# Performance work log

Hardware: AMD Instinct MI355X
Metric: run time of the kernel (lower is better)

## Reference

```python
import jax, jax.numpy as jnp
import numpy as np

N, E, M, B = 1024, 8192, 8192, 64
IN_CH, H_CH, H = 512, 1024, 8
D = H_CH // H  # 128


def setup_inputs() -> dict:
    key = jax.random.key(0)
    ks = jax.random.split(key, 16)
    inp = {
        "q": jax.random.normal(ks[0], (N, IN_CH), jnp.float32),
        "k": jax.random.normal(ks[1], (N, IN_CH), jnp.float32),
        "v": jax.random.normal(ks[2], (N, IN_CH), jnp.float32),
        "envelope": jax.random.uniform(ks[3], (M,), jnp.float32),
        "attn_bias": jax.random.normal(ks[4], (N, M), jnp.float32),
        "Wq": jax.random.normal(ks[5], (H_CH, IN_CH), jnp.float32) / np.sqrt(IN_CH),
        "bq": jnp.zeros((H_CH,), jnp.float32),
        "Wk": jax.random.normal(ks[6], (H_CH, IN_CH), jnp.float32) / np.sqrt(IN_CH),
        "bk": jnp.zeros((H_CH,), jnp.float32),
        "Wv": jax.random.normal(ks[7], (H_CH, IN_CH), jnp.float32) / np.sqrt(IN_CH),
        "bv": jnp.zeros((H_CH,), jnp.float32),
        "ln_g": jnp.ones((H_CH,), jnp.float32),
        "ln_b": jnp.zeros((H_CH,), jnp.float32),
        "Wo": jax.random.normal(ks[8], (IN_CH, H_CH), jnp.float32) / np.sqrt(H_CH),
        "bo": jnp.zeros((IN_CH,), jnp.float32),
        "atom_index": jax.random.randint(ks[9], (E,), 0, N),
        "batch_index": jnp.sort(jax.random.randint(ks[10], (E,), 0, B)),
        "edge_map_tab": jax.random.randint(ks[11], (E,), 0, M),
    }
    return inp


def reference(q, k, v, envelope, attn_bias, Wq, bq, Wk, bk, Wv, bv, ln_g, ln_b, Wo, bo,
              atom_index, batch_index, edge_map_tab):
    # projections
    qp = q @ Wq.T + bq                       # [N, H_CH]
    kp = k @ Wk.T + bk
    vp = v @ Wv.T + bv
    # edge gather of k/v
    ke = kp[atom_index].reshape(E, H, D)     # [E, H, D]
    ve = vp[atom_index].reshape(E, H, D)
    qh = qp.reshape(N, H, D)
    # scores: torch computes q*sqrt(d)/d == q/sqrt(d)
    scores = jnp.einsum('nhd,ehd->ehn', qh, ke) / jnp.sqrt(jnp.float32(D))  # [E, H, N]
    scores = scores + attn_bias[:, edge_map_tab].T[:, None, :]             # [E, 1, N]
    env_e = envelope[edge_map_tab]                                          # [E]
    # smooth scatter softmax over edges grouped by batch_index
    seg_max = jax.ops.segment_max(scores, batch_index, num_segments=B)      # [B, H, N]
    ex = jnp.exp(scores - seg_max[batch_index]) * env_e[:, None, None]
    seg_sum = jax.ops.segment_sum(ex, batch_index, num_segments=B)
    w = ex / (seg_sum[batch_index] + 1e-16)
    # second envelope weighting
    w = w * env_e[:, None, None]
    out = jnp.einsum('ehn,ehd->nhd', w, ve).reshape(N, H_CH)
    # layer norm (eps=1e-7)
    mu = out.mean(-1, keepdims=True)
    var = out.var(-1, keepdims=True)
    out = (out - mu) / jnp.sqrt(var + 1e-7) * ln_g + ln_b
    return out @ Wo.T + bo                    # [N, IN_CH]
```

## Files before the change

### kernel.cpp

```cpp
#include <hip/hip_runtime.h>
#include <hip/hip_bf16.h>
#include <math.h>

#define N_ATOMS 1024
#define E_EDGES 8192
#define M_ENV   8192
#define B_SEG   64
#define IN_CH   512
#define H_CH    1024
#define H_HEADS 8
#define D_HEAD  128

typedef __attribute__((ext_vector_type(8))) short short8_t;
typedef __attribute__((ext_vector_type(4))) float f32x4;
typedef __attribute__((ext_vector_type(4))) unsigned short ushort4_t;

__device__ __forceinline__ unsigned short f2bf(float x) {
    union { float f; unsigned u; } c; c.f = x;
    unsigned r = c.u + 0x7FFF + ((c.u >> 16) & 1);
    return (unsigned short)(r >> 16);
}
__device__ __forceinline__ float bf2f(unsigned short b) {
    union { unsigned u; float f; } c; c.u = ((unsigned)b) << 16;
    return c.f;
}

__global__ __launch_bounds__(256) void seg_offsets_k(const int* __restrict__ batch_index,
                                                     int* __restrict__ seg_off) {
    __shared__ int cnt[B_SEG];
    int t = threadIdx.x;
    if (t < B_SEG) cnt[t] = 0;
    __syncthreads();
    for (int e = t; e < E_EDGES; e += 256) {
        atomicAdd(&cnt[batch_index[e]], 1);
    }
    __syncthreads();
    if (t == 0) {
        int acc = 0;
        for (int b = 0; b < B_SEG; ++b) { seg_off[b] = acc; acc += cnt[b]; }
        seg_off[B_SEG] = acc;
    }
}

__global__ __launch_bounds__(256) void pack_k(const int* __restrict__ atom_index,
                                              const int* __restrict__ edge_map,
                                              const int* __restrict__ batch_index,
                                              const float* __restrict__ envelope,
                                              int2* __restrict__ pkenv) {
    const int e = blockIdx.x * 256 + threadIdx.x;
    const int a = atom_index[e];
    const int em = edge_map[e];
    const int bg = batch_index[e];
    int2 o;
    o.x = a | (em << 10) | (bg << 23);
    o.y = __float_as_int(envelope[em]);
    pkenv[e] = o;
}

__global__ __launch_bounds__(256) void transpose_bias_k(const float* __restrict__ ab,
                                                        unsigned short* __restrict__ abT) {
    __shared__ float tile[64][65];
    const int m0 = blockIdx.x * 64;
    const int n0 = blockIdx.y * 64;
    const int t = threadIdx.x;
    const int c4 = (t & 15) * 4;
    const int r  = t >> 4;
#pragma unroll
    for (int it = 0; it < 4; ++it) {
        const int row = r + it * 16;
        const float4 v = *(const float4*)(ab + (size_t)(n0 + row) * M_ENV + m0 + c4);
        tile[row][c4 + 0] = v.x;
        tile[row][c4 + 1] = v.y;
        tile[row][c4 + 2] = v.z;
        tile[row][c4 + 3] = v.w;
    }
    __syncthreads();
    const int mr = t >> 2;
    const int nq = t & 3;
#pragma unroll
    for (int i = 0; i < 4; ++i) {
        const int nl = nq * 4 + i * 16;
        ushort4_t o;
        o[0] = f2bf(tile[nl + 0][mr]);
        o[1] = f2bf(tile[nl + 1][mr]);
        o[2] = f2bf(tile[nl + 2][mr]);
        o[3] = f2bf(tile[nl + 3][mr]);
        *(ushort4_t*)(abT + (size_t)(m0 + mr) * N_ATOMS + n0 + nl) = o;
    }
}

struct Proj3 {
    const float* A[3];
    const float* B[3];
    const float* bia[3];
    unsigned short* C[3];
};

__global__ __launch_bounds__(256) void proj3_k(Proj3 P) {
    __shared__ unsigned short As[64 * 40];
    __shared__ unsigned short Bs[64 * 40];
    const int t = threadIdx.x;
    const int w = t >> 6, lane = t & 63, g = lane >> 4, lo = lane & 15;
    const int m0 = blockIdx.x * 64, n0 = blockIdx.y * 64;
    const int z = blockIdx.z;
    const int srow = t >> 2, sc8 = (t & 3) * 8;
    const float scale = (z == 0) ? 0.08838834764831845f : 1.0f;

    f32x4 acc[4];
#pragma unroll
    for (int nf = 0; nf < 4; ++nf) acc[nf] = (f32x4){0.f, 0.f, 0.f, 0.f};

    const float* gA = P.A[z] + (size_t)(m0 + srow) * IN_CH + sc8;
    const float* gB = P.B[z] + (size_t)(n0 + srow) * IN_CH + sc8;
    const int swr = srow * 40 + sc8;

    for (int k0 = 0; k0 < IN_CH; k0 += 32) {
        const float4 a0 = *(const float4*)(gA + k0);
        const float4 a1 = *(const float4*)(gA + k0 + 4);
        const float4 b0 = *(const float4*)(gB + k0);
        const float4 b1 = *(const float4*)(gB + k0 + 4);
        short8_t av, bvv;
        av[0]=f2bf(a0.x); av[1]=f2bf(a0.y); av[2]=f2bf(a0.z); av[3]=f2bf(a0.w);
        av[4]=f2bf(a1.x); av[5]=f2bf(a1.y); av[6]=f2bf(a1.z); av[7]=f2bf(a1.w);
        bvv[0]=f2bf(b0.x); bvv[1]=f2bf(b0.y); bvv[2]=f2bf(b0.z); bvv[3]=f2bf(b0.w);
        bvv[4]=f2bf(b1.x); bvv[5]=f2bf(b1.y); bvv[6]=f2bf(b1.z); bvv[7]=f2bf(b1.w);
        __syncthreads();
        *(short8_t*)&As[swr] = av;
        *(short8_t*)&Bs[swr] = bvv;
        __syncthreads();
        const short8_t af = *(const short8_t*)&As[(w * 16 + lo) * 40 + g * 8];
#pragma unroll
        for (int nf = 0; nf < 4; ++nf) {
            const short8_t bf = *(const short8_t*)&Bs[(nf * 16 + lo) * 40 + g * 8];
            acc[nf] = __builtin_amdgcn_mfma_f32_16x16x32_bf16(af, bf, acc[nf], 0, 0, 0);
        }
    }

#pragma unroll
    for (int nf = 0; nf < 4; ++nf) {
        const int col = n0 + nf * 16 + lo;
        const float bvv = P.bia[z][col];
#pragma unroll
        for (int r = 0; r < 4; ++r) {
            const int row = m0 + w * 16 + 4 * g + r;
            P.C[z][(size_t)row * H_CH + col] = f2bf((acc[nf][r] + bvv) * scale);
        }
    }
}

__global__ __launch_bounds__(256) void spre_k(const unsigned short* __restrict__ kb,
                                              const unsigned short* __restrict__ qb,
                                              unsigned short* __restrict__ SpT) {
    __shared__ unsigned short As[64 * 40];
    __shared__ unsigned short Bs[64 * 40];
    const int t = threadIdx.x;
    const int w = t >> 6, lane = t & 63, g = lane >> 4, lo = lane & 15;
    const int a0 = blockIdx.x * 64, n0 = blockIdx.y * 64;
    const int h = blockIdx.z;
    const int srow = t >> 2, sc8 = (t & 3) * 8;

    f32x4 acc[4];
#pragma unroll
    for (int nf = 0; nf < 4; ++nf) acc[nf] = (f32x4){0.f, 0.f, 0.f, 0.f};

    const unsigned short* gA = kb + (size_t)(a0 + srow) * H_CH + h * D_HEAD + sc8;
    const unsigned short* gB = qb + (size_t)(n0 + srow) * H_CH + h * D_HEAD + sc8;
    const int swr = srow * 40 + sc8;

#pragma unroll
    for (int k0 = 0; k0 < D_HEAD; k0 += 32) {
        const short8_t av = *(const short8_t*)(gA + k0);
        const short8_t bv = *(const short8_t*)(gB + k0);
        __syncthreads();
        *(short8_t*)&As[swr] = av;
        *(short8_t*)&Bs[swr] = bv;
        __syncthreads();
        const short8_t af = *(const short8_t*)&As[(w * 16 + lo) * 40 + g * 8];
#pragma unroll
        for (int nf = 0; nf < 4; ++nf) {
            const short8_t bf = *(const short8_t*)&Bs[(nf * 16 + lo) * 40 + g * 8];
            acc[nf] = __builtin_amdgcn_mfma_f32_16x16x32_bf16(af, bf, acc[nf], 0, 0, 0);
        }
    }

    unsigned short* dst = SpT + ((size_t)h << 20);
#pragma unroll
    for (int nf = 0; nf < 4; ++nf) {
        const int col = n0 + nf * 16 + lo;
#pragma unroll
        for (int r = 0; r < 4; ++r) {
            const int row = a0 + w * 16 + 4 * g + r;
            dst[(size_t)row * N_ATOMS + col] = f2bf(acc[nf][r]);
        }
    }
}

__global__ __launch_bounds__(256) void lsum3_k(const unsigned short* __restrict__ SpT,
                                               const unsigned short* __restrict__ abT,
                                               const int2* __restrict__ pkenv,
                                               const int* __restrict__ seg_off,
                                               unsigned short* __restrict__ rrbf) {
    __shared__ float lred[16][128];
    const int t = threadIdx.x;
    const int cslot = (t & 15) * 8;
    const int eway = t >> 4;
    const int n0 = blockIdx.x * 128;
    const int h = blockIdx.y, s = blockIdx.z;
    const unsigned short* Sh = SpT + ((size_t)h << 20);

    const int e0 = seg_off[s], e1 = seg_off[s + 1];
    float l[8] = {};

#pragma unroll 2
    for (int e = e0 + eway; e < e1; e += 16) {
        const int2 pk = pkenv[e];
        const float env = __int_as_float(pk.y);
        const int a_  = pk.x & 1023;
        const int em_ = (pk.x >> 10) & 8191;
        const short8_t su = *(const short8_t*)(Sh  + (size_t)a_  * N_ATOMS + n0 + cslot);
        const short8_t bu = *(const short8_t*)(abT + (size_t)em_ * N_ATOMS + n0 + cslot);
#pragma unroll
        for (int j = 0; j < 8; ++j)
            l[j] += __expf(bf2f((unsigned short)su[j]) + bf2f((unsigned short)bu[j])) * env;
    }
#pragma unroll
    for (int j = 0; j < 8; ++j) lred[eway][cslot + j] = l[j];
    __syncthreads();
    if (t < 128) {
        float sum = 0.f;
#pragma unroll
        for (int wv = 0; wv < 16; ++wv) sum += lred[wv][t];
        rrbf[(((size_t)h * B_SEG + s) << 10) + n0 + t] = f2bf(1.0f / (sum + 1e-16f));
    }
}

#define LGKM_BARRIER()                                          \
    do {                                                        \
        asm volatile("s_waitcnt lgkmcnt(0)" ::: "memory");      \
        __builtin_amdgcn_sched_barrier(0);                      \
        __builtin_amdgcn_s_barrier();                           \
    } while (0)

#define PV_GATHER(cc)                                                            \
    do {                                                                         \
        const int eb = ebase + (cc) * 64;                                        \
        _Pragma("unroll")                                                        \
        for (int ei = 0; ei < 2; ++ei) {                                         \
            const int e = eb + ei * 32 + (lane >> 1);                            \
            const int2 pk = pkenv[e];                                            \
            pkP[ei] = pk.x;                                                      \
            enP[ei] = __int_as_float(pk.y);                                      \
            const int a_  = pk.x & 1023;                                         \
            const int em_ = (pk.x >> 10) & 8191;                                 \
            sP[ei] = *(const short8_t*)(Sh  + (size_t)a_  * N_ATOMS + ncol8);    \
            bP[ei] = *(const short8_t*)(abT + (size_t)em_ * N_ATOMS + ncol8);    \
        }                                                                        \
        {                                                                        \
            const int eA = eb + el;                                              \
            const int aA = pkenv[eA].x & 1023;                                   \
            const int aB = pkenv[eA + 1].x & 1023;                               \
            const unsigned short* pA = vh + (size_t)aA * H_CH;                   \
            const unsigned short* pB = vh + (size_t)aB * H_CH;                   \
            vP[0] = *(const short8_t*)(pA);                                      \
            vP[1] = *(const short8_t*)(pA + 8);                                  \
            vP[2] = *(const short8_t*)(pB);                                      \
            vP[3] = *(const short8_t*)(pB + 8);                                  \
        }                                                                        \
    } while (0)

__global__ __launch_bounds__(256, 4) void pv4_k(
    const unsigned short* __restrict__ SpT,
    const unsigned short* __restrict__ vb,
    const unsigned short* __restrict__ abT,
    const int2* __restrict__ pkenv,
    const unsigned short* __restrict__ rrbf,
    unsigned short* __restrict__ part)
{
    __shared__ unsigned short plds[64][72];
    __shared__ unsigned short vst[128][72];
    __shared__ unsigned short rrlds[64 * 64];

    const int t = threadIdx.x;
    const int wid = t >> 6, lane = t & 63;
    const int g = lane >> 4, lo = lane & 15;
    const int half = lane & 1;
    const int n0 = blockIdx.x * 64;
    const int h = blockIdx.y, kc = blockIdx.z;
    const int ebase = kc * 1024;
    const int c8l = wid * 16 + half * 8;
    const int ncol8 = n0 + c8l;
    const unsigned short* Sh = SpT + ((size_t)h << 20);
    const int el = (t & 31) * 2;
    const int dh = (t >> 5) * 16;
    const unsigned short* vh = vb + h * D_HEAD + dh;

    {
        const int s_ = t >> 2;
        const int c16 = (t & 3) * 16;
        const unsigned short* src = rrbf + (((size_t)h * B_SEG + s_) << 10) + n0 + c16;
#pragma unroll
        for (int b2 = 0; b2 < 2; ++b2) {
            const int cb = (t & 3) * 2 + b2;
            const int pos = cb ^ (s_ & 7);
            *(short8_t*)&rrlds[s_ * 64 + pos * 8] = *(const short8_t*)(src + b2 * 8);
        }
    }
    __syncthreads();

    f32x4 osg[8];
#pragma unroll
    for (int di = 0; di < 8; ++di) osg[di] = (f32x4){0.f, 0.f, 0.f, 0.f};

    int pkP[2];
    short8_t sP[2], bP[2];
    float enP[2];
    short8_t vP[4];

    PV_GATHER(0);

    for (int sc = 0; sc < 16; ++sc) {
        LGKM_BARRIER();

#pragma unroll
        for (int j = 0; j < 8; ++j) {
            const int d0 = dh + j;
            const int c0 = ((((el >> 3) ^ (d0 >> 4)) & 7) << 3) + (el & 7);
            *(unsigned*)&vst[d0][c0] =
                (unsigned)(unsigned short)vP[0][j] |
                ((unsigned)(unsigned short)vP[2][j] << 16);
            const int d1 = dh + 8 + j;
            const int c1 = ((((el >> 3) ^ (d1 >> 4)) & 7) << 3) + (el & 7);
            *(unsigned*)&vst[d1][c1] =
                (unsigned)(unsigned short)vP[1][j] |
                ((unsigned)(unsigned short)vP[3][j] << 16);
        }
#pragma unroll
        for (int ei = 0; ei < 2; ++ei) {
            const int bseg = (pkP[ei] >> 23) & 63;
            const int cbr = (wid * 2 + half) ^ (bseg & 7);
            const short8_t rr8 = *(const short8_t*)&rrlds[bseg * 64 + cbr * 8];
            const float ee2 = enP[ei] * enP[ei];
            const int e_loc = ei * 32 + (lane >> 1);
#pragma unroll
            for (int j = 0; j < 8; ++j) {
                const float sv = bf2f((unsigned short)sP[ei][j]) + bf2f((unsigned short)bP[ei][j]);
                const float w_ = __expf(sv) * ee2 * bf2f((unsigned short)rr8[j]);
                plds[c8l + j][e_loc] = f2bf(w_);
            }
        }
        LGKM_BARRIER();

        if (sc + 1 < 16) PV_GATHER(sc + 1);

        const short8_t af0 = *(const short8_t*)&plds[wid * 16 + lo][g * 8];
        const short8_t af1 = *(const short8_t*)&plds[wid * 16 + lo][32 + g * 8];
        __builtin_amdgcn_s_setprio(1);
#pragma unroll
        for (int di = 0; di < 8; ++di) {
            const short8_t b0 = *(const short8_t*)&vst[di * 16 + lo][((g ^ di) & 7) << 3];
            osg[di] = __builtin_amdgcn_mfma_f32_16x16x32_bf16(af0, b0, osg[di], 0, 0, 0);
            const short8_t b1 = *(const short8_t*)&vst[di * 16 + lo][(((4 + g) ^ di) & 7) << 3];
            osg[di] = __builtin_amdgcn_mfma_f32_16x16x32_bf16(af1, b1, osg[di], 0, 0, 0);
        }
        __builtin_amdgcn_s_setprio(0);
    }

#pragma unroll
    for (int di = 0; di < 8; ++di)
#pragma unroll
        for (int r = 0; r < 4; ++r)
            part[((size_t)kc * N_ATOMS + n0 + wid * 16 + 4 * g + r) * H_CH
                 + h * D_HEAD + di * 16 + lo] = f2bf(osg[di][r]);
}

__global__ __launch_bounds__(256) void layernorm8_k(const unsigned short* __restrict__ part,
                                                    const float* __restrict__ gm,
                                                    const float* __restrict__ bt,
                                                    unsigned short* __restrict__ y) {
    const int row = blockIdx.x;
    const int t = threadIdx.x;
    const size_t base = (size_t)row * H_CH;
    float4 v = make_float4(0.f, 0.f, 0.f, 0.f);
#pragma unroll
    for (int p = 0; p < 8; ++p) {
        const ushort4_t a = ((const ushort4_t*)(part + (size_t)p * N_ATOMS * H_CH + base))[t];
        v.x += bf2f(a[0]); v.y += bf2f(a[1]); v.z += bf2f(a[2]); v.w += bf2f(a[3]);
    }

    float s  = v.x + v.y + v.z + v.w;
    float s2 = v.x * v.x + v.y * v.y + v.z * v.z + v.w * v.w;
#pragma unroll
    for (int o = 1; o < 64; o <<= 1) {
        s  += __shfl_xor(s, o);
        s2 += __shfl_xor(s2, o);
    }
    __shared__ float red[8];
    const int wid = t >> 6;
    if ((t & 63) == 0) { red[wid] = s; red[wid + 4] = s2; }
    __syncthreads();
    const float ts  = red[0] + red[1] + red[2] + red[3];
    const float ts2 = red[4] + red[5] + red[6] + red[7];

    const float mean = ts * (1.0f / (float)H_CH);
    const float var  = ts2 * (1.0f / (float)H_CH) - mean * mean;
    const float rstd = rsqrtf(var + 1e-7f);

    const float4 gv = ((const float4*)gm)[t];
    const float4 bv = ((const float4*)bt)[t];
    ushort4_t o;
    o[0] = f2bf((v.x - mean) * rstd * gv.x + bv.x);
    o[1] = f2bf((v.y - mean) * rstd * gv.y + bv.y);
    o[2] = f2bf((v.z - mean) * rstd * gv.z + bv.z);
    o[3] = f2bf((v.w - mean) * rstd * gv.w + bv.w);
    ((ushort4_t*)(y + base))[t] = o;
}

__global__ __launch_bounds__(256) void gemm_out_k(const unsigned short* __restrict__ A,
                                                  const float* __restrict__ B,
                                                  const float* __restrict__ bias,
                                                  float* __restrict__ C) {
    __shared__ unsigned short As[64 * 40];
    __shared__ unsigned short Bs[64 * 40];
    const int t = threadIdx.x;
    const int w = t >> 6, lane = t & 63, g = lane >> 4, lo = lane & 15;
    const int m0 = blockIdx.x * 64, n0 = blockIdx.y * 64;
    const int srow = t >> 2, sc8 = (t & 3) * 8;

    f32x4 acc[4];
#pragma unroll
    for (int nf = 0; nf < 4; ++nf) acc[nf] = (f32x4){0.f, 0.f, 0.f, 0.f};

    const unsigned short* gA = A + (size_t)(m0 + srow) * H_CH + sc8;
    const float* gB = B + (size_t)(n0 + srow) * H_CH + sc8;
    const int swr = srow * 40 + sc8;

    for (int k0 = 0; k0 < H_CH; k0 += 32) {
        const short8_t av = *(const short8_t*)(gA + k0);
        const float4 b0 = *(const float4*)(gB + k0);
        const float4 b1 = *(const float4*)(gB + k0 + 4);
        short8_t bvv;
        bvv[0]=f2bf(b0.x); bvv[1]=f2bf(b0.y); bvv[2]=f2bf(b0.z); bvv[3]=f2bf(b0.w);
        bvv[4]=f2bf(b1.x); bvv[5]=f2bf(b1.y); bvv[6]=f2bf(b1.z); bvv[7]=f2bf(b1.w);
        __syncthreads();
        *(short8_t*)&As[swr] = av;
        *(short8_t*)&Bs[swr] = bvv;
        __syncthreads();
        const short8_t af = *(const short8_t*)&As[(w * 16 + lo) * 40 + g * 8];
#pragma unroll
        for (int nf = 0; nf < 4; ++nf) {
            const short8_t bf = *(const short8_t*)&Bs[(nf * 16 + lo) * 40 + g * 8];
            acc[nf] = __builtin_amdgcn_mfma_f32_16x16x32_bf16(af, bf, acc[nf], 0, 0, 0);
        }
    }

#pragma unroll
    for (int nf = 0; nf < 4; ++nf) {
        const int col = n0 + nf * 16 + lo;
        const float bvv = bias[col];
#pragma unroll
        for (int r = 0; r < 4; ++r) {
            const int row = m0 + w * 16 + 4 * g + r;
            C[(size_t)row * IN_CH + col] = acc[nf][r] + bvv;
        }
    }
}

extern "C" void kernel_launch(void* const* d_in, const int* in_sizes, int n_in,
                              void* d_out, int out_size, void* d_ws, size_t ws_size,
                              hipStream_t stream) {
    (void)in_sizes; (void)n_in; (void)out_size; (void)ws_size;
    const float* q         = (const float*)d_in[0];
    const float* k         = (const float*)d_in[1];
    const float* v         = (const float*)d_in[2];
    const float* envelope  = (const float*)d_in[3];
    const float* attn_bias = (const float*)d_in[4];
    const float* Wq        = (const float*)d_in[5];
    const float* bq        = (const float*)d_in[6];
    const float* Wk        = (const float*)d_in[7];
    const float* bk        = (const float*)d_in[8];
    const float* Wv        = (const float*)d_in[9];
    const float* bv        = (const float*)d_in[10];
    const float* ln_g      = (const float*)d_in[11];
    const float* ln_b      = (const float*)d_in[12];
    const float* Wo        = (const float*)d_in[13];
    const float* bo        = (const float*)d_in[14];
    const int* atom_index  = (const int*)d_in[15];
    const int* batch_index = (const int*)d_in[16];
    const int* edge_map    = (const int*)d_in[17];
    float* out = (float*)d_out;

    char* w8 = (char*)d_ws;
    unsigned short* SpT   = (unsigned short*)(w8);
    unsigned short* abT   = (unsigned short*)(w8 + (16u << 20));
    unsigned short* partb = (unsigned short*)(w8 + (32u << 20));
    unsigned short* vbuf  = (unsigned short*)(w8 + (48u << 20));
    unsigned short* qb    = (unsigned short*)(w8 + (50u << 20));
    unsigned short* kb    = (unsigned short*)(w8 + (52u << 20));
    unsigned short* ln_o  = (unsigned short*)(w8 + (54u << 20));
    unsigned short* rrbf  = (unsigned short*)(w8 + (56u << 20));
    int2*           pkenv = (int2*)          (w8 + (58u << 20));
    int*            seg   = (int*)           (w8 + (59u << 20));

    seg_offsets_k<<<1, 256, 0, stream>>>(batch_index, seg);
    pack_k<<<E_EDGES / 256, 256, 0, stream>>>(atom_index, edge_map, batch_index,
                                              envelope, pkenv);
    transpose_bias_k<<<dim3(M_ENV / 64, N_ATOMS / 64), 256, 0, stream>>>(attn_bias, abT);

    Proj3 pj;
    pj.A[0] = q;   pj.A[1] = k;   pj.A[2] = v;
    pj.B[0] = Wq;  pj.B[1] = Wk;  pj.B[2] = Wv;
    pj.bia[0] = bq; pj.bia[1] = bk; pj.bia[2] = bv;
    pj.C[0] = qb;  pj.C[1] = kb;  pj.C[2] = vbuf;
    proj3_k<<<dim3(16, 16, 3), 256, 0, stream>>>(pj);

    spre_k<<<dim3(16, 16, H_HEADS), 256, 0, stream>>>(kb, qb, SpT);

    lsum3_k<<<dim3(8, H_HEADS, B_SEG), 256, 0, stream>>>(SpT, abT, pkenv, seg, rrbf);

    pv4_k<<<dim3(N_ATOMS / 64, H_HEADS, 8), 256, 0, stream>>>(
        SpT, vbuf, abT, pkenv, rrbf, partb);

    layernorm8_k<<<N_ATOMS, 256, 0, stream>>>(partb, ln_g, ln_b, ln_o);

    gemm_out_k<<<dim3(16, 8), 256, 0, stream>>>(ln_o, Wo, bo, out);
}
```

Before: 170.1 us.

## Double-buffer PV gathers two chunks ahead, swizzle P tile, shuffle V indices

The PV kernel now keeps two register sets of gathered edge data, so each chunk's global loads are issued two chunks before they are consumed rather than one. The P tile in LDS gets an XOR column swizzle to cut bank conflicts on the scattered writes and fragment reads. The atom indices for the V gather are taken by wave shuffles from already loaded pack data instead of reloading pkenv from global memory. The extra register set raises VGPR pressure, which could hurt occupancy under the 4-blocks launch bound.

```diff
diff --git a/kernel.cpp b/kernel.cpp
--- a/kernel.cpp
+++ b/kernel.cpp
@@ -241,34 +241,88 @@
         __builtin_amdgcn_s_barrier();                           \
     } while (0)
 
-#define PV_GATHER(cc)                                                            \
+#define PV_GATHER(pkX, sX, bX, enX, vX, cc)                                      \
     do {                                                                         \
-        const int eb = ebase + (cc) * 64;                                        \
+        const int eb_ = ebase + (cc) * 64;                                       \
         _Pragma("unroll")                                                        \
         for (int ei = 0; ei < 2; ++ei) {                                         \
-            const int e = eb + ei * 32 + (lane >> 1);                            \
+            const int e = eb_ + ei * 32 + (lane >> 1);                           \
             const int2 pk = pkenv[e];                                            \
-            pkP[ei] = pk.x;                                                      \
-            enP[ei] = __int_as_float(pk.y);                                      \
+            pkX[ei] = pk.x;                                                      \
+            enX[ei] = __int_as_float(pk.y);                                      \
             const int a_  = pk.x & 1023;                                         \
             const int em_ = (pk.x >> 10) & 8191;                                 \
-            sP[ei] = *(const short8_t*)(Sh  + (size_t)a_  * N_ATOMS + ncol8);    \
-            bP[ei] = *(const short8_t*)(abT + (size_t)em_ * N_ATOMS + ncol8);    \
+            sX[ei] = *(const short8_t*)(Sh  + (size_t)a_  * N_ATOMS + ncol8);    \
+            bX[ei] = *(const short8_t*)(abT + (size_t)em_ * N_ATOMS + ncol8);    \
         }                                                                        \
         {                                                                        \
-            const int eA = eb + el;                                              \
-            const int aA = pkenv[eA].x & 1023;                                   \
-            const int aB = pkenv[eA + 1].x & 1023;                               \
+              \
+            const int sl0 = (el & 31) * 2;                                       \
+            const int va00 = __shfl(pkX[0], sl0);                                \
+            const int va01 = __shfl(pkX[1], sl0);                                \
+            const int va10 = __shfl(pkX[0], sl0 + 2);                            \
+            const int va11 = __shfl(pkX[1], sl0 + 2);                            \
+            const int aA = ((el < 32) ? va00 : va01) & 1023;                     \
+            const int aB = ((el < 32) ? va10 : va11) & 1023;                     \
             const unsigned short* pA = vh + (size_t)aA * H_CH;                   \
             const unsigned short* pB = vh + (size_t)aB * H_CH;                   \
-            vP[0] = *(const short8_t*)(pA);                                      \
-            vP[1] = *(const short8_t*)(pA + 8);                                  \
-            vP[2] = *(const short8_t*)(pB);                                      \
-            vP[3] = *(const short8_t*)(pB + 8);                                  \
+            vX[0] = *(const short8_t*)(pA);                                      \
+            vX[1] = *(const short8_t*)(pA + 8);                                  \
+            vX[2] = *(const short8_t*)(pB);                                      \
+            vX[3] = *(const short8_t*)(pB + 8);                                  \
         }                                                                        \
     } while (0)
 
-__global__ __launch_bounds__(256, 4) void pv4_k(
+#define PV_CONSUME(pkX, sX, bX, enX, vX)                                         \
+    do {                                                                         \
+        _Pragma("unroll")                                                        \
+        for (int j = 0; j < 8; ++j) {                                            \
+            const int d0 = dh + j;                                               \
+            const int c0 = ((((el >> 3) ^ (d0 >> 4)) & 7) << 3) + (el & 7);      \
+            *(unsigned*)&vst[d0][c0] =                                           \
+                (unsigned)(unsigned short)vX[0][j] |                             \
+                ((unsigned)(unsigned short)vX[2][j] << 16);                      \
+            const int d1 = dh + 8 + j;                                           \
+            const int c1 = ((((el >> 3) ^ (d1 >> 4)) & 7) << 3) + (el & 7);      \
+            *(unsigned*)&vst[d1][c1] =                                           \
+                (unsigned)(unsigned short)vX[1][j] |                             \
+                ((unsigned)(unsigned short)vX[3][j] << 16);                      \
+        }                                                                        \
+        _Pragma("unroll")                                                        \
+        for (int ei = 0; ei < 2; ++ei) {                                         \
+            const int bseg = (pkX[ei] >> 23) & 63;                               \
+            const int cbr = (wid * 2 + half) ^ (bseg & 7);                       \
+            const short8_t rr8 = *(const short8_t*)&rrlds[bseg * 64 + cbr * 8];  \
+            const float ee2 = enX[ei] * enX[ei];                                 \
+            const int E = ei * 32 + (lane >> 1);                                 \
+            const int ecol = (((E >> 3) ^ rowx) << 3) | (E & 7);                 \
+            _Pragma("unroll")                                                    \
+            for (int j = 0; j < 8; ++j) {                                        \
+                const float sv = bf2f((unsigned short)sX[ei][j]) + bf2f((unsigned short)bX[ei][j]); \
+                const float w_ = __expf(sv) * ee2 * bf2f((unsigned short)rr8[j]);\
+                plds[c8l + j][ecol] = f2bf(w_);                                  \
+            }                                                                    \
+        }                                                                        \
+    } while (0)
+
+#define PV_MFMA()                                                                \
+    do {                                                                         \
+        const int arow = wid * 16 + lo;                                          \
+        const int arx = (2 * wid + (lo >> 3)) & 7;                               \
+        const short8_t af0 = *(const short8_t*)&plds[arow][(g ^ arx) << 3];      \
+        const short8_t af1 = *(const short8_t*)&plds[arow][((4 + g) ^ arx) << 3];\
+        __builtin_amdgcn_s_setprio(1);                                           \
+        _Pragma("unroll")                                                        \
+        for (int di = 0; di < 8; ++di) {                                         \
+            const short8_t b0 = *(const short8_t*)&vst[di * 16 + lo][((g ^ di) & 7) << 3]; \
+            osg[di] = __builtin_amdgcn_mfma_f32_16x16x32_bf16(af0, b0, osg[di], 0, 0, 0);  \
+            const short8_t b1 = *(const short8_t*)&vst[di * 16 + lo][(((4 + g) ^ di) & 7) << 3]; \
+            osg[di] = __builtin_amdgcn_mfma_f32_16x16x32_bf16(af1, b1, osg[di], 0, 0, 0);  \
+        }                                                                        \
+        __builtin_amdgcn_s_setprio(0);                                           \
+    } while (0)
+
+__global__ __launch_bounds__(256, 4) void pv5_k(
     const unsigned short* __restrict__ SpT,
     const unsigned short* __restrict__ vb,
     const unsigned short* __restrict__ abT,
@@ -288,9 +342,10 @@
     const int h = blockIdx.y, kc = blockIdx.z;
     const int ebase = kc * 1024;
     const int c8l = wid * 16 + half * 8;
+    const int rowx = (2 * wid + half) & 7;
     const int ncol8 = n0 + c8l;
     const unsigned short* Sh = SpT + ((size_t)h << 20);
-    const int el = (t & 31) * 2;
+    const int el = (lane & 31) * 2;
     const int dh = (t >> 5) * 16;
     const unsigned short* vh = vb + h * D_HEAD + dh;
 
@@ -311,58 +366,26 @@
 #pragma unroll
     for (int di = 0; di < 8; ++di) osg[di] = (f32x4){0.f, 0.f, 0.f, 0.f};
 
-    int pkP[2];
-    short8_t sP[2], bP[2];
-    float enP[2];
-    short8_t vP[4];
-
-    PV_GATHER(0);
-
-    for (int sc = 0; sc < 16; ++sc) {
+    int pkA[2], pkB[2];
+    short8_t sA[2], bA[2], vA[4];
+    short8_t sB[2], bB[2], vB[4];
+    float enA[2], enB[2];
+
+    PV_GATHER(pkA, sA, bA, enA, vA, 0);
+    PV_GATHER(pkB, sB, bB, enB, vB, 1);
+
+#pragma unroll 1
+    for (int cp = 0; cp < 8; ++cp) {
         LGKM_BARRIER();
-
-#pragma unroll
-        for (int j = 0; j < 8; ++j) {
-            const int d0 = dh + j;
-            const int c0 = ((((el >> 3) ^ (d0 >> 4)) & 7) << 3) + (el & 7);
-            *(unsigned*)&vst[d0][c0] =
-                (unsigned)(unsigned short)vP[0][j] |
-                ((unsigned)(unsigned short)vP[2][j] << 16);
-            const int d1 = dh + 8 + j;
-            const int c1 = ((((el >> 3) ^ (d1 >> 4)) & 7) << 3) + (el & 7);
-            *(unsigned*)&vst[d1][c1] =
-                (unsigned)(unsigned short)vP[1][j] |
-                ((unsigned)(unsigned short)vP[3][j] << 16);
-        }
-#pragma unroll
-        for (int ei = 0; ei < 2; ++ei) {
-            const int bseg = (pkP[ei] >> 23) & 63;
-            const int cbr = (wid * 2 + half) ^ (bseg & 7);
-            const short8_t rr8 = *(const short8_t*)&rrlds[bseg * 64 + cbr * 8];
-            const float ee2 = enP[ei] * enP[ei];
-            const int e_loc = ei * 32 + (lane >> 1);
-#pragma unroll
-            for (int j = 0; j < 8; ++j) {
-                const float sv = bf2f((unsigned short)sP[ei][j]) + bf2f((unsigned short)bP[ei][j]);
-                const float w_ = __expf(sv) * ee2 * bf2f((unsigned short)rr8[j]);
-                plds[c8l + j][e_loc] = f2bf(w_);
-            }
-        }
+        PV_CONSUME(pkA, sA, bA, enA, vA);
         LGKM_BARRIER();
-
-        if (sc + 1 < 16) PV_GATHER(sc + 1);
-
-        const short8_t af0 = *(const short8_t*)&plds[wid * 16 + lo][g * 8];
-        const short8_t af1 = *(const short8_t*)&plds[wid * 16 + lo][32 + g * 8];
-        __builtin_amdgcn_s_setprio(1);
-#pragma unroll
-        for (int di = 0; di < 8; ++di) {
-            const short8_t b0 = *(const short8_t*)&vst[di * 16 + lo][((g ^ di) & 7) << 3];
-            osg[di] = __builtin_amdgcn_mfma_f32_16x16x32_bf16(af0, b0, osg[di], 0, 0, 0);
-            const short8_t b1 = *(const short8_t*)&vst[di * 16 + lo][(((4 + g) ^ di) & 7) << 3];
-            osg[di] = __builtin_amdgcn_mfma_f32_16x16x32_bf16(af1, b1, osg[di], 0, 0, 0);
-        }
-        __builtin_amdgcn_s_setprio(0);
+        if (cp < 7) PV_GATHER(pkA, sA, bA, enA, vA, 2 * cp + 2);
+        PV_MFMA();
+        LGKM_BARRIER();
+        PV_CONSUME(pkB, sB, bB, enB, vB);
+        LGKM_BARRIER();
+        if (cp < 7) PV_GATHER(pkB, sB, bB, enB, vB, 2 * cp + 3);
+        PV_MFMA();
     }
 
 #pragma unroll
@@ -517,7 +540,7 @@
 
     lsum3_k<<<dim3(8, H_HEADS, B_SEG), 256, 0, stream>>>(SpT, abT, pkenv, seg, rrbf);
 
-    pv4_k<<<dim3(N_ATOMS / 64, H_HEADS, 8), 256, 0, stream>>>(
+    pv5_k<<<dim3(N_ATOMS / 64, H_HEADS, 8), 256, 0, stream>>>(
         SpT, vbuf, abT, pkenv, rrbf, partb);
 
     layernorm8_k<<<N_ATOMS, 256, 0, stream>>>(partb, ln_g, ln_b, ln_o);
```

Result: slower. 197.9 us (+16.3%).
